# Performance work log

Measured on AMD Instinct MI355X. Metric: run time of the kernel, lower is better.

Reference implementation:

```python
import jax, jax.numpy as jnp
import numpy as np

B, H, W, C = 4, 64, 64, 1280
NH = 16          # num heads
HD = C // NH     # 80 features per head
WS = 14          # window size
REL = 2 * WS - 1 # 27 relative-position entries per axis
EPS = 1e-6


def setup_inputs() -> dict:
    key = jax.random.key(0)
    ks = jax.random.split(key, 16)
    s = 0.02
    return {
        "imagelike_bhwc": jax.random.normal(ks[0], (B, H, W, C), jnp.float32),
        "ln1_g": jnp.ones((C,), jnp.float32),
        "ln1_b": jnp.zeros((C,), jnp.float32),
        "qkv_w": jax.random.normal(ks[1], (C, 3 * C), jnp.float32) * s,
        "qkv_b": jnp.zeros((3 * C,), jnp.float32),
        "proj_w": jax.random.normal(ks[2], (C, C), jnp.float32) * s,
        "proj_b": jnp.zeros((C,), jnp.float32),
        "rel_pos_h": jax.random.normal(ks[3], (REL, HD), jnp.float32) * s,
        "rel_pos_w": jax.random.normal(ks[4], (REL, HD), jnp.float32) * s,
        "ln2_g": jnp.ones((C,), jnp.float32),
        "ln2_b": jnp.zeros((C,), jnp.float32),
        "mlp_w1": jax.random.normal(ks[5], (C, 4 * C), jnp.float32) * s,
        "mlp_b1": jnp.zeros((4 * C,), jnp.float32),
        "mlp_w2": jax.random.normal(ks[6], (4 * C, C), jnp.float32) * s,
        "mlp_b2": jnp.zeros((C,), jnp.float32),
    }


def _layernorm(t, g, b):
    mu = jnp.mean(t, axis=-1, keepdims=True)
    var = jnp.var(t, axis=-1, keepdims=True)
    return (t - mu) * jax.lax.rsqrt(var + EPS) * g + b


def reference(imagelike_bhwc, ln1_g, ln1_b, qkv_w, qkv_b, proj_w, proj_b,
              rel_pos_h, rel_pos_w, ln2_g, ln2_b, mlp_w1, mlp_b1, mlp_w2, mlp_b2):
    x = imagelike_bhwc
    b, h, w, c = x.shape
    hd = c // NH
    scale = hd ** -0.5
    # --- image -> windows (pad to multiple of WS) ---
    hp, wp = (-h) % WS, (-w) % WS
    xp = jnp.pad(x, ((0, 0), (0, hp), (0, wp), (0, 0)))
    Hp, Wp = h + hp, w + wp
    ny, nx = Hp // WS, Wp // WS
    win = xp.reshape(b, ny, WS, nx, WS, c).transpose(0, 1, 3, 2, 4, 5)
    win = win.reshape(b * ny * nx, WS, WS, c)      # (Bw, S, S, C)
    Bw, N = win.shape[0], WS * WS
    # --- pre-attention layernorm + qkv ---
    t = _layernorm(win, ln1_g, ln1_b)
    qkv = t.reshape(Bw, N, c) @ qkv_w + qkv_b      # (Bw, N, 3C)
    qkv = qkv.reshape(Bw, N, 3, NH, hd).transpose(2, 0, 3, 1, 4)  # (3,Bw,NH,N,hd)
    q, k, v = qkv[0], qkv[1], qkv[2]
    # --- scores + decomposed relative position bias ---
    attn = jnp.einsum('bhqd,bhkd->bhqk', q * scale, k)            # (Bw,NH,N,N)
    idx = jnp.arange(WS)[:, None] - jnp.arange(WS)[None, :] + (WS - 1)
    Rh = rel_pos_h[idx]                                           # (WS,WS,hd)
    Rw = rel_pos_w[idx]                                           # (WS,WS,hd)
    qr = q.reshape(Bw, NH, WS, WS, hd)
    bias_h = jnp.einsum('bnyxd,ykd->bnyxk', qr, Rh)               # (Bw,NH,WS,WS,WS)
    bias_w = jnp.einsum('bnyxd,xkd->bnyxk', qr, Rw)
    bias = (bias_h[..., :, None] + bias_w[..., None, :]).reshape(Bw, NH, N, N)
    attn = jax.nn.softmax(attn + bias, axis=-1)
    out = jnp.einsum('bhqk,bhkd->bhqd', attn, v)                  # (Bw,NH,N,hd)
    out = out.transpose(0, 2, 1, 3).reshape(Bw, WS, WS, c)
    out = out @ proj_w + proj_b
    attn_out = out + win                                          # residual 1
    # --- MLP ---
    t2 = _layernorm(attn_out, ln2_g, ln2_b)
    mlp = jax.nn.gelu(t2 @ mlp_w1 + mlp_b1, approximate=False) @ mlp_w2 + mlp_b2
    out = mlp + attn_out                                          # residual 2
    # --- windows -> image (remove padding) ---
    img = out.reshape(b, ny, nx, WS, WS, c).transpose(0, 1, 3, 2, 4, 5)
    img = img.reshape(b, Hp, Wp, c)
    return img[:, :h, :w, :]
```

## Files before the change

### kernel.cpp

```cpp
#include <hip/hip_runtime.h>

typedef __attribute__((ext_vector_type(8))) short short8;
typedef __attribute__((ext_vector_type(4))) float f32x4;

#define GLBP(p) ((const __attribute__((address_space(1))) void*)(p))
#define LDSP(p) ((__attribute__((address_space(3))) void*)(p))

__device__ __forceinline__ float bf2f(unsigned short u) {
  return __uint_as_float(((unsigned int)u) << 16);
}
__device__ __forceinline__ unsigned short f2bf(float f) {
  unsigned int u = __float_as_uint(f);
  u += 0x7fff + ((u >> 16) & 1);
  return (unsigned short)(u >> 16);
}

__device__ __forceinline__ void tok2pix(int gt, int& b, int& py, int& px) {
  int w = gt / 196, t = gt - w * 196;
  b = w / 25;
  int wr = w - b * 25;
  int wy = wr / 5, wx = wr - wy * 5;
  int ty = t / 14;
  py = wy * 14 + ty;
  px = wx * 14 + (t - ty * 14);
}

__global__ void k_transpose(const float* __restrict__ W, unsigned short* __restrict__ Wt,
                            int K, int N) {
  __shared__ float tile[32][33];
  int tx = threadIdx.x, ty = threadIdx.y;
  int n0 = blockIdx.x * 32, k0 = blockIdx.y * 32;
#pragma unroll
  for (int i = 0; i < 4; ++i)
    tile[ty + 8 * i][tx] = W[(size_t)(k0 + ty + 8 * i) * N + n0 + tx];
  __syncthreads();
#pragma unroll
  for (int i = 0; i < 4; ++i)
    Wt[(size_t)(n0 + ty + 8 * i) * K + k0 + tx] = f2bf(tile[tx][ty + 8 * i]);
}

__global__ __launch_bounds__(256) void k_ln1(const float* __restrict__ x,
                                             const float* __restrict__ g,
                                             const float* __restrict__ be,
                                             unsigned short* __restrict__ A1,
                                             int w0, int ctok) {
  int m = blockIdx.x * 4 + (threadIdx.x >> 6);
  int lane = threadIdx.x & 63;
  int b, py, px;
  tok2pix(w0 * 196 + m, b, py, px);
  bool valid = (m < ctok) && (py < 64) && (px < 64);
  const float* row = x + ((size_t)((b * 64 + py) * 64 + px)) * 1280;
  float v[20];
#pragma unroll
  for (int i = 0; i < 20; ++i) v[i] = valid ? row[lane + 64 * i] : 0.f;
  float s = 0.f, ss = 0.f;
#pragma unroll
  for (int i = 0; i < 20; ++i) { s += v[i]; ss += v[i] * v[i]; }
#pragma unroll
  for (int o = 32; o > 0; o >>= 1) { s += __shfl_down(s, o); ss += __shfl_down(ss, o); }
  s = __shfl(s, 0);
  ss = __shfl(ss, 0);
  float mu = s * (1.f / 1280.f);
  float var = ss * (1.f / 1280.f) - mu * mu;
  float rinv = rsqrtf(var + 1e-6f);
  unsigned short* o1 = A1 + (size_t)m * 1280;
#pragma unroll
  for (int i = 0; i < 20; ++i) {
    int c = lane + 64 * i;
    o1[c] = f2bf((v[i] - mu) * rinv * g[c] + be[c]);
  }
}

__global__ __launch_bounds__(256) void k_ln2(const unsigned short* __restrict__ AT,
                                             const float* __restrict__ g,
                                             const float* __restrict__ be,
                                             unsigned short* __restrict__ A2) {
  int m = blockIdx.x * 4 + (threadIdx.x >> 6);
  int lane = threadIdx.x & 63;
  const unsigned short* row = AT + (size_t)m * 1280;
  float v[20];
#pragma unroll
  for (int i = 0; i < 20; ++i) v[i] = bf2f(row[lane + 64 * i]);
  float s = 0.f, ss = 0.f;
#pragma unroll
  for (int i = 0; i < 20; ++i) { s += v[i]; ss += v[i] * v[i]; }
#pragma unroll
  for (int o = 32; o > 0; o >>= 1) { s += __shfl_down(s, o); ss += __shfl_down(ss, o); }
  s = __shfl(s, 0);
  ss = __shfl(ss, 0);
  float mu = s * (1.f / 1280.f);
  float var = ss * (1.f / 1280.f) - mu * mu;
  float rinv = rsqrtf(var + 1e-6f);
  unsigned short* o1 = A2 + (size_t)m * 1280;
#pragma unroll
  for (int i = 0; i < 20; ++i) {
    int c = lane + 64 * i;
    o1[c] = f2bf((v[i] - mu) * rinv * g[c] + be[c]);
  }
}

template <int EPI>
__device__ __forceinline__ void gemm_body(const unsigned short* __restrict__ A,
                                          const unsigned short* __restrict__ Bt,
                                          int K, int N, int gx,
                                          const float* __restrict__ bias,
                                          void* __restrict__ outp,
                                          const float* __restrict__ xres,
                                          const unsigned short* __restrict__ attnres,
                                          int w0, int ctok) {
  __shared__ __align__(16) char smem[73728];
  int tid = threadIdx.x;
  int w = tid >> 6, lane = tid & 63;
  int nwg = gridDim.x, bid = blockIdx.x;
  int q = nwg >> 3, r = nwg & 7;
  int xcd = bid & 7, loc = bid >> 3;
  int wg = (xcd < r ? xcd * (q + 1) : r * (q + 1) + (xcd - r) * q) + loc;
  int bx = wg % gx, by = wg / gx;
  int mBase = by * 256, nBase = bx * 128;
  int wr = w >> 2, wc = w & 3;
  int la = lane & 15, lg = lane >> 4;

  int srow = tid >> 2;
  int schunk = (tid & 3) ^ ((srow >> 1) & 3);
  const char* pa0 = (const char*)A + (size_t)(mBase + srow) * K * 2 + (schunk << 4);
  const char* pa1 = (const char*)A + (size_t)(mBase + 128 + srow) * K * 2 + (schunk << 4);
  const char* pb0 = (const char*)Bt + (size_t)(nBase + srow) * K * 2 + (schunk << 4);
  int ldst = tid * 16;

  auto STAGE = [&](int slot, size_t ko) {
    int b = slot * 24576;
    __builtin_amdgcn_global_load_lds(GLBP(pa0 + ko), LDSP(smem + b + ldst), 16, 0, 0);
    __builtin_amdgcn_global_load_lds(GLBP(pa1 + ko), LDSP(smem + b + 8192 + ldst), 16, 0, 0);
    __builtin_amdgcn_global_load_lds(GLBP(pb0 + ko), LDSP(smem + b + 16384 + ldst), 16, 0, 0);
  };

  int offA[8], offB[2];
#pragma unroll
  for (int m = 0; m < 8; ++m) {
    int rr = wr * 128 + m * 16 + la;
    offA[m] = rr * 64 + ((lg ^ ((rr >> 1) & 3)) << 4);
  }
#pragma unroll
  for (int n = 0; n < 2; ++n) {
    int rr = wc * 32 + n * 16 + la;
    offB[n] = 16384 + rr * 64 + ((lg ^ ((rr >> 1) & 3)) << 4);
  }

  const f32x4 z4 = {0.f, 0.f, 0.f, 0.f};
  f32x4 acc[8][2];
#pragma unroll
  for (int m = 0; m < 8; ++m)
#pragma unroll
    for (int n = 0; n < 2; ++n) acc[m][n] = z4;

  int NT = K >> 5;
  STAGE(0, 0);
  STAGE(1, 64);
  int rs = 0;
  for (int t = 0; t < NT; ++t) {
    if (t + 1 < NT)
      asm volatile("s_waitcnt vmcnt(3)" ::: "memory");
    else
      asm volatile("s_waitcnt vmcnt(0)" ::: "memory");
    __builtin_amdgcn_s_barrier();
    __builtin_amdgcn_sched_barrier(0);
    if (t + 2 < NT) {
      int ws = rs + 2;
      if (ws >= 3) ws -= 3;
      STAGE(ws, (size_t)(t + 2) * 64);
    }
    const char* buf = (const char*)smem + rs * 24576;
    short8 af[4], bfr[2];
#pragma unroll
    for (int n = 0; n < 2; ++n) bfr[n] = *(const short8*)(buf + offB[n]);
#pragma unroll
    for (int m = 0; m < 4; ++m) af[m] = *(const short8*)(buf + offA[m]);
    __builtin_amdgcn_s_setprio(1);
#pragma unroll
    for (int m = 0; m < 4; ++m)
#pragma unroll
      for (int n = 0; n < 2; ++n)
        acc[m][n] = __builtin_amdgcn_mfma_f32_16x16x32_bf16(af[m], bfr[n], acc[m][n], 0, 0, 0);
    __builtin_amdgcn_s_setprio(0);
    __builtin_amdgcn_sched_barrier(0);
#pragma unroll
    for (int m = 0; m < 4; ++m) af[m] = *(const short8*)(buf + offA[m + 4]);
    __builtin_amdgcn_s_setprio(1);
#pragma unroll
    for (int m = 0; m < 4; ++m)
#pragma unroll
      for (int n = 0; n < 2; ++n)
        acc[m + 4][n] = __builtin_amdgcn_mfma_f32_16x16x32_bf16(af[m], bfr[n], acc[m + 4][n], 0, 0, 0);
    __builtin_amdgcn_s_setprio(0);
    rs = (rs == 2) ? 0 : rs + 1;
  }

#pragma unroll
  for (int m = 0; m < 8; ++m) {
#pragma unroll
    for (int n = 0; n < 2; ++n) {
      int col = nBase + wc * 32 + n * 16 + la;
      float bcol = bias[col];
#pragma unroll
      for (int j = 0; j < 4; ++j) {
        int row = mBase + wr * 128 + m * 16 + lg * 4 + j;
        float v = acc[m][n][j] + bcol;
        if (EPI == 0) {
          if (row < ctok) {
            int wloc = row / 196, tt = row - wloc * 196;
            int which = col / 1280, cr = col - which * 1280;
            int nh = cr / 80, d = cr - nh * 80;
            ((unsigned short*)outp)[((((size_t)wloc * 16 + nh) * 3 + which) * 196 + tt) * 80 + d] =
                f2bf(v);
          }
        } else if (EPI == 2) {
          float gg = 0.5f * v * (1.f + erff(v * 0.70710678118654752f));
          ((unsigned short*)outp)[(size_t)row * N + col] = f2bf(gg);
        } else if (EPI == 1) {
          if (row < ctok) {
            int b, py, px;
            tok2pix(w0 * 196 + row, b, py, px);
            float wv = (py < 64 && px < 64)
                           ? xres[((size_t)((b * 64 + py) * 64 + px)) * 1280 + col]
                           : 0.f;
            ((unsigned short*)outp)[(size_t)row * 1280 + col] = f2bf(v + wv);
          }
        } else {
          if (row < ctok) {
            int b, py, px;
            tok2pix(w0 * 196 + row, b, py, px);
            if (py < 64 && px < 64)
              ((float*)outp)[((size_t)((b * 64 + py) * 64 + px)) * 1280 + col] =
                  v + bf2f(attnres[(size_t)row * 1280 + col]);
          }
        }
      }
    }
  }
}

__global__ __launch_bounds__(512, 4) void k_gqkv(const unsigned short* A, const unsigned short* Bt,
                                                 int K, int N, int gx, const float* bias, void* o,
                                                 const float* xr, const unsigned short* ar, int w0, int ct) {
  gemm_body<0>(A, Bt, K, N, gx, bias, o, xr, ar, w0, ct);
}
__global__ __launch_bounds__(512, 4) void k_gproj(const unsigned short* A, const unsigned short* Bt,
                                                  int K, int N, int gx, const float* bias, void* o,
                                                  const float* xr, const unsigned short* ar, int w0, int ct) {
  gemm_body<1>(A, Bt, K, N, gx, bias, o, xr, ar, w0, ct);
}
__global__ __launch_bounds__(512, 4) void k_gmlp1(const unsigned short* A, const unsigned short* Bt,
                                                  int K, int N, int gx, const float* bias, void* o,
                                                  const float* xr, const unsigned short* ar, int w0, int ct) {
  gemm_body<2>(A, Bt, K, N, gx, bias, o, xr, ar, w0, ct);
}
__global__ __launch_bounds__(512, 4) void k_gmlp2(const unsigned short* A, const unsigned short* Bt,
                                                  int K, int N, int gx, const float* bias, void* o,
                                                  const float* xr, const unsigned short* ar, int w0, int ct) {
  gemm_body<3>(A, Bt, K, N, gx, bias, o, xr, ar, w0, ct);
}

__global__ __launch_bounds__(256) void k_relbias(const unsigned short* __restrict__ qkv,
                                                 const float* __restrict__ rph,
                                                 const float* __restrict__ rpw,
                                                 unsigned short* __restrict__ B) {
  int wh = blockIdx.x;
  const unsigned short* qb = qkv + (size_t)wh * 47040;
  for (int id = threadIdx.x; id < 196 * 28; id += 256) {
    int t = id / 28, c = id - t * 28;
    int y = t / 14, xx = t - y * 14;
    const float* R = (c < 14) ? (rph + (size_t)(y - c + 13) * 80)
                              : (rpw + (size_t)(xx - (c - 14) + 13) * 80);
    const unsigned short* qq = qb + (size_t)t * 80;
    float acc = 0.f;
#pragma unroll
    for (int d8 = 0; d8 < 10; ++d8) {
      short8 qv = *(const short8*)(qq + d8 * 8);
      const float4* Rv = (const float4*)(R + d8 * 8);
      float4 ra = Rv[0], rb = Rv[1];
      acc += bf2f((unsigned short)qv[0]) * ra.x + bf2f((unsigned short)qv[1]) * ra.y +
             bf2f((unsigned short)qv[2]) * ra.z + bf2f((unsigned short)qv[3]) * ra.w +
             bf2f((unsigned short)qv[4]) * rb.x + bf2f((unsigned short)qv[5]) * rb.y +
             bf2f((unsigned short)qv[6]) * rb.z + bf2f((unsigned short)qv[7]) * rb.w;
    }
    B[(size_t)wh * 5488 + id] = f2bf(acc);
  }
}

__global__ __launch_bounds__(256, 2) void k_attn(const unsigned short* __restrict__ qkv,
                                                 const unsigned short* __restrict__ Bias,
                                                 unsigned short* __restrict__ AO) {
  __shared__ unsigned short Vt[80 * 232];
  __shared__ unsigned short Ps[4][16 * 232];
  __shared__ unsigned short Bls[196 * 28];
  int bid = blockIdx.x;
  int half = bid & 1, wh = bid >> 1;
  int w = wh >> 4, nh = wh & 15;
  int tid = threadIdx.x, wid = tid >> 6, lane = tid & 63;
  int la = lane & 15, lg = lane >> 4;
  const unsigned short* qb = qkv + (size_t)wh * 47040;
  const unsigned short* kb = qb + 15680;
  const unsigned short* vb = qb + 31360;
  const short8 z8 = {0, 0, 0, 0, 0, 0, 0, 0};

  for (int c = tid; c < 1960; c += 256) {
    int t = c / 10, d8 = (c - t * 10) * 8;
    short8 vv = *(const short8*)(vb + (size_t)t * 80 + d8);
#pragma unroll
    for (int e = 0; e < 8; ++e) Vt[(d8 + e) * 232 + t] = (unsigned short)vv[e];
  }
  for (int i = tid; i < 80 * 36; i += 256) Vt[(i / 36) * 232 + 196 + (i % 36)] = 0;
  for (int i = tid; i < 686; i += 256)
    ((short8*)Bls)[i] = ((const short8*)(Bias + (size_t)wh * 5488))[i];
  __syncthreads();

  int kyv[13], kxv[13];
#pragma unroll
  for (int ci = 0; ci < 13; ++ci) {
    int key = ci * 16 + la;
    kyv[ci] = key / 14;
    kxv[ci] = key - kyv[ci] * 14;
  }

  const float scale = 0.111803398874989485f;
  const f32x4 z4 = {0.f, 0.f, 0.f, 0.f};
  unsigned short* P = Ps[wid];

  auto process = [&](int rb) {
    short8 qa[3];
#pragma unroll
    for (int kk = 0; kk < 3; ++kk) {
      int d = kk * 32 + lg * 8;
      qa[kk] = (kk < 2 || lg < 2) ? *(const short8*)(qb + (size_t)(rb * 16 + la) * 80 + d) : z8;
    }
    f32x4 s[13];
#pragma unroll
    for (int i = 0; i < 13; ++i) s[i] = z4;
#pragma unroll
    for (int kk = 0; kk < 3; ++kk) {
      int d = kk * 32 + lg * 8;
#pragma unroll
      for (int ni = 0; ni < 13; ++ni) {
        short8 bb = *(const short8*)(kb + (size_t)(ni * 16 + la) * 80 + d);
        s[ni] = __builtin_amdgcn_mfma_f32_16x16x32_bf16(qa[kk], bb, s[ni], 0, 0, 0);
      }
    }
#pragma unroll
    for (int j = 0; j < 4; ++j) {
      int rloc = lg * 4 + j;
      int t = rb * 16 + rloc;
      bool tval = t < 196;
      const unsigned short* Bp = Bls + (tval ? t : 0) * 28;
      float v[13];
      float mx = -3e30f;
#pragma unroll
      for (int ci = 0; ci < 13; ++ci) {
        int key = ci * 16 + la;
        float val = s[ci][j] * scale;
        if (key < 196 && tval) val += bf2f(Bp[kyv[ci]]) + bf2f(Bp[14 + kxv[ci]]);
        if (key >= 196 || !tval) val = -3e30f;
        v[ci] = val;
        mx = fmaxf(mx, val);
      }
#pragma unroll
      for (int o = 1; o < 16; o <<= 1) mx = fmaxf(mx, __shfl_xor(mx, o));
      float sum = 0.f;
#pragma unroll
      for (int ci = 0; ci < 13; ++ci) {
        float e = __expf(v[ci] - mx);
        v[ci] = e;
        sum += e;
      }
#pragma unroll
      for (int o = 1; o < 16; o <<= 1) sum += __shfl_xor(sum, o);
      float inv = 1.f / sum;
#pragma unroll
      for (int ci = 0; ci < 13; ++ci) P[rloc * 232 + ci * 16 + la] = f2bf(v[ci] * inv);
      P[rloc * 232 + 208 + la] = 0;
    }
    f32x4 o5[5];
#pragma unroll
    for (int i = 0; i < 5; ++i) o5[i] = z4;
#pragma unroll
    for (int kc = 0; kc < 7; ++kc) {
      short8 aa = *(const short8*)(P + la * 232 + kc * 32 + lg * 8);
#pragma unroll
      for (int ni = 0; ni < 5; ++ni) {
        short8 bb = *(const short8*)(Vt + (ni * 16 + la) * 232 + kc * 32 + lg * 8);
        o5[ni] = __builtin_amdgcn_mfma_f32_16x16x32_bf16(aa, bb, o5[ni], 0, 0, 0);
      }
    }
#pragma unroll
    for (int ni = 0; ni < 5; ++ni)
#pragma unroll
      for (int j = 0; j < 4; ++j) {
        int t = rb * 16 + lg * 4 + j;
        if (t < 196)
          AO[((size_t)w * 196 + t) * 1280 + nh * 80 + ni * 16 + la] = f2bf(o5[ni][j]);
      }
  };

  if (half == 0) {
    process(wid);
    if (wid < 3) process(wid + 4);
  } else {
    process(7 + wid);
    if (wid < 2) process(11 + wid);
  }
}

extern "C" void kernel_launch(void* const* d_in, const int* in_sizes, int n_in,
                              void* d_out, int out_size, void* d_ws, size_t ws_size,
                              hipStream_t stream) {
  const float* x = (const float*)d_in[0];
  const float* ln1g = (const float*)d_in[1];
  const float* ln1b = (const float*)d_in[2];
  const float* qkvw = (const float*)d_in[3];
  const float* qkvb = (const float*)d_in[4];
  const float* projw = (const float*)d_in[5];
  const float* projb = (const float*)d_in[6];
  const float* rph = (const float*)d_in[7];
  const float* rpw = (const float*)d_in[8];
  const float* ln2g = (const float*)d_in[9];
  const float* ln2b = (const float*)d_in[10];
  const float* w1 = (const float*)d_in[11];
  const float* b1 = (const float*)d_in[12];
  const float* w2 = (const float*)d_in[13];
  const float* b2 = (const float*)d_in[14];
  float* out = (float*)d_out;

  const size_t woff = (3840ull * 1280 + 1280ull * 1280 + 5120ull * 1280 + 1280ull * 5120) * 2;
  const int NWopts[10] = {25, 20, 16, 12, 10, 8, 5, 4, 2, 1};
  int NW = 0, Mb = 0;
  for (int i = 0; i < 10; ++i) {
    int nw = NWopts[i];
    int mb = ((nw * 196 + 255) / 256) * 256;
    size_t tot = woff + (size_t)mb * 15360 + (size_t)nw * 16 * 5488 * 2;
    if (tot <= ws_size) { NW = nw; Mb = mb; break; }
  }
  if (!NW) return;

  char* p = (char*)d_ws;
  unsigned short* qkvwT = (unsigned short*)p; p += 3840ull * 1280 * 2;
  unsigned short* projwT = (unsigned short*)p; p += 1280ull * 1280 * 2;
  unsigned short* w1T = (unsigned short*)p; p += 5120ull * 1280 * 2;
  unsigned short* w2T = (unsigned short*)p; p += 1280ull * 5120 * 2;
  unsigned short* A1 = (unsigned short*)p; p += (size_t)Mb * 2560;
  unsigned short* QKV = (unsigned short*)p; p += (size_t)Mb * 7680;
  unsigned short* AO = (unsigned short*)p; p += (size_t)Mb * 2560;
  unsigned short* ATTN = (unsigned short*)p; p += (size_t)Mb * 2560;
  unsigned short* BIAS = (unsigned short*)p;
  unsigned short* Hb = QKV;
  unsigned short* A2 = A1;

  k_transpose<<<dim3(120, 40), dim3(32, 8), 0, stream>>>(qkvw, qkvwT, 1280, 3840);
  k_transpose<<<dim3(40, 40), dim3(32, 8), 0, stream>>>(projw, projwT, 1280, 1280);
  k_transpose<<<dim3(160, 40), dim3(32, 8), 0, stream>>>(w1, w1T, 1280, 5120);
  k_transpose<<<dim3(40, 160), dim3(32, 8), 0, stream>>>(w2, w2T, 5120, 1280);

  int gy = Mb / 256;
  int nchunks = (100 + NW - 1) / NW;
  for (int c = 0; c < nchunks; ++c) {
    int w0 = c * NW;
    int cw = (100 - w0 < NW) ? (100 - w0) : NW;
    int ctok = cw * 196;
    k_ln1<<<Mb / 4, 256, 0, stream>>>(x, ln1g, ln1b, A1, w0, ctok);
    k_gqkv<<<30 * gy, 512, 0, stream>>>(A1, qkvwT, 1280, 3840, 30, qkvb, (void*)QKV,
                                        nullptr, nullptr, 0, ctok);
    k_relbias<<<cw * 16, 256, 0, stream>>>(QKV, rph, rpw, BIAS);
    k_attn<<<cw * 32, 256, 0, stream>>>(QKV, BIAS, AO);
    k_gproj<<<10 * gy, 512, 0, stream>>>(AO, projwT, 1280, 1280, 10, projb, (void*)ATTN,
                                         x, nullptr, w0, ctok);
    k_ln2<<<Mb / 4, 256, 0, stream>>>(ATTN, ln2g, ln2b, A2);
    k_gmlp1<<<40 * gy, 512, 0, stream>>>(A2, w1T, 1280, 5120, 40, b1, (void*)Hb,
                                         nullptr, nullptr, 0, ctok);
    k_gmlp2<<<10 * gy, 512, 0, stream>>>(Hb, w2T, 5120, 1280, 10, b2, (void*)out,
                                         nullptr, ATTN, w0, ctok);
  }
}
```

Measured before the change: 1.899 ms.

## Fuse relative-position bias into attention kernel via augmented QK MFMA

Merges the separate rel-bias kernel into the attention kernel, so each block of 512 threads handles one window-head and computes the bias table in LDS. K is stored pre-scaled in a swizzled LDS buffer and extended with one-hot columns, and Q is extended with the bias values, so the bias add is done by an extra MFMA k-step instead of per-element gathers. This removes a launch and the global round trip of the bias buffer. In exchange it uses more LDS per block (about one block per CU), quantizes the scaled K and the bias to bf16, and gives up the two-blocks-per-head split.

```diff
diff --git a/kernel.cpp b/kernel.cpp
--- a/kernel.cpp
+++ b/kernel.cpp
@@ -260,13 +260,52 @@
   gemm_body<3>(A, Bt, K, N, gx, bias, o, xr, ar, w0, ct);
 }
 
-__global__ __launch_bounds__(256) void k_relbias(const unsigned short* __restrict__ qkv,
+__global__ __launch_bounds__(512, 1) void k_attn(const unsigned short* __restrict__ qkv,
                                                  const float* __restrict__ rph,
                                                  const float* __restrict__ rpw,
-                                                 unsigned short* __restrict__ B) {
+                                                 unsigned short* __restrict__ AO) {
+  __shared__ unsigned short Ks[208 * 128];
+  __shared__ unsigned short Vt[80 * 232];
+  __shared__ unsigned short Ps[8][16 * 232];
+  __shared__ unsigned short Bls[196 * 28];
   int wh = blockIdx.x;
+  int w = wh >> 4, nh = wh & 15;
+  int tid = threadIdx.x, wid = tid >> 6, lane = tid & 63;
+  int la = lane & 15, lg = lane >> 4;
   const unsigned short* qb = qkv + (size_t)wh * 47040;
-  for (int id = threadIdx.x; id < 196 * 28; id += 256) {
+  const unsigned short* kb = qb + 15680;
+  const unsigned short* vb = qb + 31360;
+  const short8 z8 = {0, 0, 0, 0, 0, 0, 0, 0};
+  const float scale = 0.111803398874989485f;
+
+  for (int c = tid; c < 208 * 16; c += 512) {
+    int t = c >> 4, seg = c & 15;
+    short8 kv = z8;
+    if (t < 196) {
+      if (seg < 10) {
+        short8 raw = *(const short8*)(kb + (size_t)t * 80 + seg * 8);
+#pragma unroll
+        for (int e = 0; e < 8; ++e)
+          kv[e] = (short)f2bf(bf2f((unsigned short)raw[e]) * scale);
+      } else if (seg < 14) {
+        int ky = t / 14, kx = t - ky * 14;
+#pragma unroll
+        for (int e = 0; e < 8; ++e) {
+          int col = seg * 8 + e;
+          kv[e] = (col == 80 + ky || col == 94 + kx) ? (short)0x3F80 : (short)0;
+        }
+      }
+    }
+    *(short8*)((char*)Ks + t * 256 + ((seg * 16) ^ ((t & 7) << 4))) = kv;
+  }
+  for (int c = tid; c < 1960; c += 512) {
+    int t = c / 10, d8 = (c - t * 10) * 8;
+    short8 vv = *(const short8*)(vb + (size_t)t * 80 + d8);
+#pragma unroll
+    for (int e = 0; e < 8; ++e) Vt[(d8 + e) * 232 + t] = (unsigned short)vv[e];
+  }
+  for (int i = tid; i < 80 * 36; i += 512) Vt[(i / 36) * 232 + 196 + (i % 36)] = 0;
+  for (int id = tid; id < 196 * 28; id += 512) {
     int t = id / 28, c = id - t * 28;
     int y = t / 14, xx = t - y * 14;
     const float* R = (c < 14) ? (rph + (size_t)(y - c + 13) * 80)
@@ -283,82 +322,65 @@
              bf2f((unsigned short)qv[4]) * rb.x + bf2f((unsigned short)qv[5]) * rb.y +
              bf2f((unsigned short)qv[6]) * rb.z + bf2f((unsigned short)qv[7]) * rb.w;
     }
-    B[(size_t)wh * 5488 + id] = f2bf(acc);
-  }
-}
-
-__global__ __launch_bounds__(256, 2) void k_attn(const unsigned short* __restrict__ qkv,
-                                                 const unsigned short* __restrict__ Bias,
-                                                 unsigned short* __restrict__ AO) {
-  __shared__ unsigned short Vt[80 * 232];
-  __shared__ unsigned short Ps[4][16 * 232];
-  __shared__ unsigned short Bls[196 * 28];
-  int bid = blockIdx.x;
-  int half = bid & 1, wh = bid >> 1;
-  int w = wh >> 4, nh = wh & 15;
-  int tid = threadIdx.x, wid = tid >> 6, lane = tid & 63;
-  int la = lane & 15, lg = lane >> 4;
-  const unsigned short* qb = qkv + (size_t)wh * 47040;
-  const unsigned short* kb = qb + 15680;
-  const unsigned short* vb = qb + 31360;
-  const short8 z8 = {0, 0, 0, 0, 0, 0, 0, 0};
-
-  for (int c = tid; c < 1960; c += 256) {
-    int t = c / 10, d8 = (c - t * 10) * 8;
-    short8 vv = *(const short8*)(vb + (size_t)t * 80 + d8);
-#pragma unroll
-    for (int e = 0; e < 8; ++e) Vt[(d8 + e) * 232 + t] = (unsigned short)vv[e];
-  }
-  for (int i = tid; i < 80 * 36; i += 256) Vt[(i / 36) * 232 + 196 + (i % 36)] = 0;
-  for (int i = tid; i < 686; i += 256)
-    ((short8*)Bls)[i] = ((const short8*)(Bias + (size_t)wh * 5488))[i];
+    Bls[id] = f2bf(acc);
+  }
   __syncthreads();
 
-  int kyv[13], kxv[13];
-#pragma unroll
-  for (int ci = 0; ci < 13; ++ci) {
-    int key = ci * 16 + la;
-    kyv[ci] = key / 14;
-    kxv[ci] = key - kyv[ci] * 14;
-  }
-
-  const float scale = 0.111803398874989485f;
   const f32x4 z4 = {0.f, 0.f, 0.f, 0.f};
   unsigned short* P = Ps[wid];
 
   auto process = [&](int rb) {
-    short8 qa[3];
-#pragma unroll
-    for (int kk = 0; kk < 3; ++kk) {
-      int d = kk * 32 + lg * 8;
-      qa[kk] = (kk < 2 || lg < 2) ? *(const short8*)(qb + (size_t)(rb * 16 + la) * 80 + d) : z8;
+    int t = rb * 16 + la;
+    bool tv = t < 196;
+    short8 qa[4];
+#pragma unroll
+    for (int kk = 0; kk < 2; ++kk)
+      qa[kk] = tv ? *(const short8*)(qb + (size_t)t * 80 + kk * 32 + lg * 8) : z8;
+    if (tv && lg < 2) {
+      qa[2] = *(const short8*)(qb + (size_t)t * 80 + 64 + lg * 8);
+    } else if (tv) {
+      short8 rr = z8;
+      int base = (lg - 2) * 8;
+#pragma unroll
+      for (int e = 0; e < 8; ++e) rr[e] = (short)Bls[t * 28 + base + e];
+      qa[2] = rr;
+    } else {
+      qa[2] = z8;
+    }
+    {
+      short8 rr = z8;
+      if (tv && lg == 0) {
+#pragma unroll
+        for (int e = 0; e < 8; ++e) rr[e] = (short)Bls[t * 28 + 16 + e];
+      } else if (tv && lg == 1) {
+#pragma unroll
+        for (int e = 0; e < 4; ++e) rr[e] = (short)Bls[t * 28 + 24 + e];
+      }
+      qa[3] = rr;
     }
     f32x4 s[13];
 #pragma unroll
     for (int i = 0; i < 13; ++i) s[i] = z4;
 #pragma unroll
-    for (int kk = 0; kk < 3; ++kk) {
-      int d = kk * 32 + lg * 8;
+    for (int kk = 0; kk < 4; ++kk) {
+      int coff = (kk * 64 + lg * 16) ^ ((la & 7) << 4);
 #pragma unroll
       for (int ni = 0; ni < 13; ++ni) {
-        short8 bb = *(const short8*)(kb + (size_t)(ni * 16 + la) * 80 + d);
+        short8 bb = *(const short8*)((char*)Ks + (ni * 16 + la) * 256 + coff);
         s[ni] = __builtin_amdgcn_mfma_f32_16x16x32_bf16(qa[kk], bb, s[ni], 0, 0, 0);
       }
     }
 #pragma unroll
     for (int j = 0; j < 4; ++j) {
       int rloc = lg * 4 + j;
-      int t = rb * 16 + rloc;
-      bool tval = t < 196;
-      const unsigned short* Bp = Bls + (tval ? t : 0) * 28;
+      int tt = rb * 16 + rloc;
+      bool ttv = tt < 196;
       float v[13];
       float mx = -3e30f;
 #pragma unroll
       for (int ci = 0; ci < 13; ++ci) {
         int key = ci * 16 + la;
-        float val = s[ci][j] * scale;
-        if (key < 196 && tval) val += bf2f(Bp[kyv[ci]]) + bf2f(Bp[14 + kxv[ci]]);
-        if (key >= 196 || !tval) val = -3e30f;
+        float val = (key < 196 && ttv) ? s[ci][j] : -3e30f;
         v[ci] = val;
         mx = fmaxf(mx, val);
       }
@@ -394,19 +416,14 @@
     for (int ni = 0; ni < 5; ++ni)
 #pragma unroll
       for (int j = 0; j < 4; ++j) {
-        int t = rb * 16 + lg * 4 + j;
-        if (t < 196)
-          AO[((size_t)w * 196 + t) * 1280 + nh * 80 + ni * 16 + la] = f2bf(o5[ni][j]);
+        int to = rb * 16 + lg * 4 + j;
+        if (to < 196)
+          AO[((size_t)w * 196 + to) * 1280 + nh * 80 + ni * 16 + la] = f2bf(o5[ni][j]);
       }
   };
 
-  if (half == 0) {
-    process(wid);
-    if (wid < 3) process(wid + 4);
-  } else {
-    process(7 + wid);
-    if (wid < 2) process(11 + wid);
-  }
+  process(wid);
+  if (wid < 5) process(wid + 8);
 }
 
 extern "C" void kernel_launch(void* const* d_in, const int* in_sizes, int n_in,
@@ -435,7 +452,7 @@
   for (int i = 0; i < 10; ++i) {
     int nw = NWopts[i];
     int mb = ((nw * 196 + 255) / 256) * 256;
-    size_t tot = woff + (size_t)mb * 15360 + (size_t)nw * 16 * 5488 * 2;
+    size_t tot = woff + (size_t)mb * 15360;
     if (tot <= ws_size) { NW = nw; Mb = mb; break; }
   }
   if (!NW) return;
@@ -448,8 +465,7 @@
   unsigned short* A1 = (unsigned short*)p; p += (size_t)Mb * 2560;
   unsigned short* QKV = (unsigned short*)p; p += (size_t)Mb * 7680;
   unsigned short* AO = (unsigned short*)p; p += (size_t)Mb * 2560;
-  unsigned short* ATTN = (unsigned short*)p; p += (size_t)Mb * 2560;
-  unsigned short* BIAS = (unsigned short*)p;
+  unsigned short* ATTN = (unsigned short*)p;
   unsigned short* Hb = QKV;
   unsigned short* A2 = A1;
 
@@ -467,8 +483,7 @@
     k_ln1<<<Mb / 4, 256, 0, stream>>>(x, ln1g, ln1b, A1, w0, ctok);
     k_gqkv<<<30 * gy, 512, 0, stream>>>(A1, qkvwT, 1280, 3840, 30, qkvb, (void*)QKV,
                                         nullptr, nullptr, 0, ctok);
-    k_relbias<<<cw * 16, 256, 0, stream>>>(QKV, rph, rpw, BIAS);
-    k_attn<<<cw * 32, 256, 0, stream>>>(QKV, BIAS, AO);
+    k_attn<<<cw * 16, 512, 0, stream>>>(QKV, rph, rpw, AO);
     k_gproj<<<10 * gy, 512, 0, stream>>>(AO, projwT, 1280, 1280, 10, projb, (void*)ATTN,
                                          x, nullptr, w0, ctok);
     k_ln2<<<Mb / 4, 256, 0, stream>>>(ATTN, ln2g, ln2b, A2);
```

After: 1.803 ms. -5.1%, faster.
